# Kernel tuning notes

Measured on AMD Instinct MI355X. Metric: run time of the kernel, lower is better.

The kernel has to match this reference:

```python
import jax, jax.numpy as jnp
import numpy as np

IN, H, L, T = 44, 128, 4, 50  # input_size, hidden_size, num_layers, target_len
B, S = 2048, 200


def _lstm_cell(xt, h, c, Wih, Whh, b):
    # xt [B,in], h/c [B,H]; Wih [4H,in], Whh [4H,H], b [4H] (b_ih+b_hh fused)
    gates = xt @ Wih.T + h @ Whh.T + b
    i, f, g, o = jnp.split(gates, 4, axis=-1)
    c_new = jax.nn.sigmoid(f) * c + jax.nn.sigmoid(i) * jnp.tanh(g)
    h_new = jax.nn.sigmoid(o) * jnp.tanh(c_new)
    return h_new, c_new


def _run_layer(xs, Wih, Whh, b):
    # xs [S,B,in] -> ys [S,B,H], final (h,c)
    Bn = xs.shape[1]
    h0 = jnp.zeros((Bn, H), xs.dtype)
    c0 = jnp.zeros((Bn, H), xs.dtype)

    def step(carry, xt):
        h, c = carry
        h, c = _lstm_cell(xt, h, c, Wih, Whh, b)
        return (h, c), h

    (hT, cT), ys = jax.lax.scan(step, (h0, c0), xs)
    return ys, hT, cT


def setup_inputs() -> dict:
    key = jax.random.key(0)
    ks = jax.random.split(key, 16)
    s = 1.0 / np.sqrt(H)
    u = lambda k, shape: jax.random.uniform(k, shape, jnp.float32, -s, s)
    return {
        "x": jax.random.normal(ks[0], (B, S, IN), jnp.float32),
        "target": jax.random.normal(ks[1], (B, T, IN), jnp.float32),
        "enc_Wih0": u(ks[2], (4 * H, IN)),
        "enc_WihR": u(ks[3], (L - 1, 4 * H, H)),
        "enc_Whh": u(ks[4], (L, 4 * H, H)),
        "enc_b": u(ks[5], (L, 4 * H)),
        "dec_Wih0": u(ks[6], (4 * H, IN)),
        "dec_WihR": u(ks[7], (L - 1, 4 * H, H)),
        "dec_Whh": u(ks[8], (L, 4 * H, H)),
        "dec_b": u(ks[9], (L, 4 * H)),
        "fc_W": u(ks[10], (IN, H)),
        "fc_b": u(ks[11], (IN,)),
    }


def reference(x, target, enc_Wih0, enc_WihR, enc_Whh, enc_b,
              dec_Wih0, dec_WihR, dec_Whh, dec_b, fc_W, fc_b):
    # ---- encoder: 4-layer LSTM over the source sequence ----
    xs = jnp.transpose(x, (1, 0, 2))  # [S,B,IN]
    ys, h, c = _run_layer(xs, enc_Wih0, enc_Whh[0], enc_b[0])
    hs, cs = [h], [c]
    for l in range(1, L):
        ys, h, c = _run_layer(ys, enc_WihR[l - 1], enc_Whh[l], enc_b[l])
        hs.append(h)
        cs.append(c)
    hs = jnp.stack(hs)  # [L,B,H]
    cs = jnp.stack(cs)

    # ---- decoder: recursive decode for T steps (seq_len=1 per step) ----
    dec_in0 = x[:, -1, :]  # [B,IN]

    def dec_step(carry, _):
        dec_in, hsc, csc = carry
        new_h, new_c = [], []
        inp = dec_in
        for l in range(L):
            Wih = dec_Wih0 if l == 0 else dec_WihR[l - 1]
            hl, cl = _lstm_cell(inp, hsc[l], csc[l], Wih, dec_Whh[l], dec_b[l])
            new_h.append(hl)
            new_c.append(cl)
            inp = hl
        out = inp @ fc_W.T + fc_b  # [B,IN]
        return (out, jnp.stack(new_h), jnp.stack(new_c)), out

    _, outs = jax.lax.scan(dec_step, (dec_in0, hs, cs), None, length=T)
    return jnp.transpose(outs, (1, 0, 2))  # [B,T,IN]
```

## Files before the change

kernel.cpp:

```cpp
#include <hip/hip_runtime.h>
#include <hip/hip_bf16.h>
#include <cstdint>
#include <cstddef>

typedef _Float16 half8  __attribute__((ext_vector_type(8)));
typedef float    floatx4 __attribute__((ext_vector_type(4)));
typedef int      int4v   __attribute__((ext_vector_type(4)));

#define S_LEN 200
#define BATCH 2048
#define HID   128
#define T_LEN 50
#define IN_D  44

#define SENT32 0x7E007E00

#define OFF_ENCW   0ull
#define OFF_DECW   983040ull
#define OFF_RING_E 1978368ull
#define OFF_RING_D 14561280ull
#define OFF_ORING  20852736ull
#define OFF_HENC   21901312ull
#define OFF_CENC   23998464ull
#define OFF_FLAGS  28192768ull

#define SCOPE_AGENT __HIP_MEMORY_SCOPE_AGENT

#define LOG2E  1.44269504f
#define LOG2E2 2.88539008f
__device__ __forceinline__ float sigf(float x){
  float e = __builtin_amdgcn_exp2f(-LOG2E * x);
  return __builtin_amdgcn_rcpf(1.f + e);
}
__device__ __forceinline__ float tanhf_fast(float x){
  float e = __builtin_amdgcn_exp2f(LOG2E2 * x);
  return 1.f - 2.f * __builtin_amdgcn_rcpf(e + 1.f);
}

__device__ __forceinline__ int  ldc(const int* p){ return __hip_atomic_load(p, __ATOMIC_RELAXED, SCOPE_AGENT); }
__device__ __forceinline__ void stc(int* p, int v){ __hip_atomic_store(p, v, __ATOMIC_RELAXED, SCOPE_AGENT); }
__device__ __forceinline__ void drain_vm(){ asm volatile("s_waitcnt vmcnt(0)" ::: "memory"); }
__device__ __forceinline__ int* flagp(int* flags, int idx){ return flags + idx*32; }

__device__ __forceinline__ int4v ld_ring_x4(const int* p){
  int4v r;
  asm volatile("global_load_dwordx4 %0, %1, off sc0 sc1\n\t"
               "s_waitcnt vmcnt(0)"
               : "=v"(r) : "v"(p) : "memory");
  return r;
}
__device__ __forceinline__ void ld_ring_x4x2(int4v &r0, int4v &r1,
                                             const int* p0, const int* p1){
  asm volatile("global_load_dwordx4 %0, %2, off sc0 sc1\n\t"
               "global_load_dwordx4 %1, %3, off sc0 sc1\n\t"
               "s_waitcnt vmcnt(0)"
               : "=&v"(r0), "=&v"(r1)
               : "v"(p0), "v"(p1)
               : "memory");
}
__device__ __forceinline__ void st_ring_x4(int* p, int4v v){
  asm volatile("global_store_dwordx4 %0, %1, off sc0 sc1"
               :: "v"(p), "v"(v) : "memory");
}
__device__ __forceinline__ bool any_sent(int4v v){
  return (v.x==SENT32)||(v.y==SENT32)||(v.z==SENT32)||(v.w==SENT32);
}

#define PIN(v) asm volatile("" : "+v"(v))

__global__ void prep_weights(const float* __restrict__ eW0, const float* __restrict__ eWR,
                             const float* __restrict__ eWH, const float* __restrict__ dW0,
                             const float* __restrict__ dWR, const float* __restrict__ dWH,
                             const float* __restrict__ fcW,
                             _Float16* __restrict__ encw, _Float16* __restrict__ decw,
                             int* __restrict__ rings, int* __restrict__ flags)
{
  int i = blockIdx.x*256 + threadIdx.x;
  if (i < 491520) {
    _Float16 v;
    if (i < 32768)      { int j=i>>6, k=i&63; v = (k<IN_D)? (_Float16)eW0[j*IN_D+k] : (_Float16)0.f; }
    else if (i < 229376){ v = (_Float16)eWR[i-32768]; }
    else                { v = (_Float16)eWH[i-229376]; }
    encw[i] = v;
  }
  if (i < 497664) {
    _Float16 v;
    if (i < 32768)      { int j=i>>6, k=i&63; v = (k<IN_D)? (_Float16)dW0[j*IN_D+k] : (_Float16)0.f; }
    else if (i < 229376){ v = (_Float16)dWR[i-32768]; }
    else if (i < 491520){ v = (_Float16)dWH[i-229376]; }
    else { int r=i-491520; int j=r>>7, k=r&127; v = (j<IN_D)? (_Float16)fcW[j*HID+k] : (_Float16)0.f; }
    decw[i] = v;
  }
  for (int j = i; j < 4980736; j += 4096*256) rings[j] = SENT32;
  if (i < 32768) flags[i] = 0;
}


__global__ __launch_bounds__(512, 2)
void enc_pipe(const float* __restrict__ x, const _Float16* __restrict__ encw,
              const float* __restrict__ enc_b, _Float16* __restrict__ ring,
              _Float16* __restrict__ h_enc, float* __restrict__ c_enc,
              int* __restrict__ flags)
{
  const int tid = threadIdx.x;
  const int w = tid >> 6, lane = tid & 63, quad = lane >> 4, n16 = lane & 15;
  const int l = blockIdx.x >> 6, s = blockIdx.x & 63, r0 = s * 32;
  const int u = w*16 + n16;
  const int KSI = (l == 0) ? 2 : 4;
  const int my4 = tid*4;

  __shared__ _Float16 xb[2][32][136];
  __shared__ _Float16 hA[32][136];
  __shared__ _Float16 hB[32][136];

  for (int i = tid; i < 32*136; i += 512){
    ((_Float16*)xb[0])[i] = (_Float16)0.f;
    ((_Float16*)xb[1])[i] = (_Float16)0.f;
    ((_Float16*)hA)[i] = (_Float16)0.f;
    ((_Float16*)hB)[i] = (_Float16)0.f;
  }

  const _Float16* Wi = (l==0) ? encw : encw + 32768 + (size_t)(l-1)*65536;
  const _Float16* Wh = encw + 229376 + (size_t)l*65536;
  const int KI = KSI * 32;
  floatx4 wfi[4][4], wfh[4][4];
  #pragma unroll
  for (int nt = 0; nt < 4; ++nt){
    const int grow = nt*128 + u;
    #pragma unroll
    for (int ks = 0; ks < 4; ++ks){
      if (ks < KSI){ wfi[nt][ks] = *(const floatx4*)(Wi + (size_t)grow*KI + ks*32 + quad*8); PIN(wfi[nt][ks]); }
      wfh[nt][ks] = *(const floatx4*)(Wh + (size_t)grow*HID + ks*32 + quad*8); PIN(wfh[nt][ks]);
    }
  }
  float breg[4];
  #pragma unroll
  for (int g = 0; g < 4; ++g) breg[g] = enc_b[l*512 + g*128 + u];
  float creg[2][4] = {{0.f,0.f,0.f,0.f},{0.f,0.f,0.f,0.f}};

  int xr_r[3], xr_k[3]; bool xr_v[3]; float xr[2][3];
  if (l == 0){
    #pragma unroll
    for (int j = 0; j < 3; ++j){
      int idx = tid + j*512; xr_v[j] = idx < 32*IN_D;
      xr_r[j] = xr_v[j] ? idx / IN_D : 0; xr_k[j] = xr_v[j] ? idx % IN_D : 0;
      #pragma unroll
      for (int p = 0; p < 2; ++p)
        xr[p][j] = xr_v[j] ? x[((size_t)(r0+xr_r[j])*S_LEN + p)*IN_D + xr_k[j]] : 0.f;
    }
  }

  int* cflag_self = flagp(flags, l*64 + s);
  int* cflag_next = flagp(flags, (l+1)*64 + s);
  int seen_cons = 0;

  auto cell = [&](const _Float16 (*xin)[136], const _Float16 (*hin)[136],
                  _Float16 (*hout)[136], bool writeHC){
    #pragma unroll
    for (int m = 0; m < 2; ++m){
      half8 ai[4], ah[4];
      #pragma unroll
      for (int ks = 0; ks < 4; ++ks){
        if (ks < KSI) ai[ks] = *(const half8*)&xin[m*16+n16][ks*32 + quad*8];
        ah[ks] = *(const half8*)&hin[m*16+n16][ks*32 + quad*8];
      }
      floatx4 acc[4];
      #pragma unroll
      for (int nt = 0; nt < 4; ++nt){
        acc[nt] = (floatx4){0.f,0.f,0.f,0.f};
        #pragma unroll
        for (int ks = 0; ks < 4; ++ks){
          if (ks < KSI) acc[nt] = __builtin_amdgcn_mfma_f32_16x16x32_f16(ai[ks], __builtin_bit_cast(half8, wfi[nt][ks]), acc[nt], 0,0,0);
          acc[nt] = __builtin_amdgcn_mfma_f32_16x16x32_f16(ah[ks], __builtin_bit_cast(half8, wfh[nt][ks]), acc[nt], 0,0,0);
        }
      }
      #pragma unroll
      for (int rr = 0; rr < 4; ++rr){
        float ip = acc[0][rr] + breg[0];
        float fp = acc[1][rr] + breg[1];
        float gp = acc[2][rr] + breg[2];
        float op = acc[3][rr] + breg[3];
        float cc = sigf(fp)*creg[m][rr] + sigf(ip)*tanhf_fast(gp);
        float hh = sigf(op)*tanhf_fast(cc);
        creg[m][rr] = cc;
        const int row = m*16 + quad*4 + rr;
        hout[row][u] = (_Float16)hh;
        if (writeHC){
          h_enc[((size_t)l*BATCH + r0 + row)*HID + u] = (_Float16)hh;
          c_enc[((size_t)l*BATCH + r0 + row)*HID + u] = cc;
        }
      }
    }
  };

  __syncthreads();

  const int4v sv = {SENT32, SENT32, SENT32, SENT32};

  for (int q = 0; q < S_LEN/2; ++q){
    if (l == 0){
      #pragma unroll
      for (int p = 0; p < 2; ++p)
        #pragma unroll
        for (int j = 0; j < 3; ++j)
          if (xr_v[j]) xb[p][xr_r[j]][xr_k[j]] = (_Float16)xr[p][j];
    } else {
      const int sbase = (l-1)*8 + ((q&3)<<1);
      int* s0 = (int*)(ring + ((size_t)(sbase+0)*BATCH + r0)*HID) + my4;
      int* s1 = (int*)(ring + ((size_t)(sbase+1)*BATCH + r0)*HID) + my4;
      int4v v0, v1;
      ld_ring_x4x2(v0, v1, s0, s1);
      while (any_sent(v0)){ __builtin_amdgcn_s_sleep(1); v0 = ld_ring_x4(s0); }
      while (any_sent(v1)){ __builtin_amdgcn_s_sleep(1); v1 = ld_ring_x4(s1); }
      *(int4v*)&xb[0][my4>>6][(my4&63)*2] = v0;
      *(int4v*)&xb[1][my4>>6][(my4&63)*2] = v1;
      st_ring_x4(s0, sv);
      st_ring_x4(s1, sv);
    }
    if (tid == 0 && l < 3 && q >= 4){
      while (seen_cons < q-3){
        seen_cons = ldc(cflag_next);
        if (seen_cons < q-3) __builtin_amdgcn_s_sleep(1);
      }
    }
    __syncthreads();

    if (l == 0 && q < S_LEN/2 - 1){
      #pragma unroll
      for (int p = 0; p < 2; ++p)
        #pragma unroll
        for (int j = 0; j < 3; ++j)
          if (xr_v[j]) xr[p][j] = x[((size_t)(r0+xr_r[j])*S_LEN + (2*q+2+p))*IN_D + xr_k[j]];
    }

    cell(xb[0], hA, hB, false);
    __syncthreads();
    if (l < 3){
      const int dbase = l*8 + ((q&3)<<1);
      int* d0p = (int*)(ring + ((size_t)(dbase+0)*BATCH + r0)*HID) + my4;
      st_ring_x4(d0p, *(const int4v*)&hB[my4>>6][(my4&63)*2]);
    }
    cell(xb[1], hB, hA, (q == S_LEN/2 - 1));
    __syncthreads();

    if (l > 0){
      drain_vm();
      if (tid == 0) stc(cflag_self, q+1);
    }
    if (l < 3){
      const int dbase = l*8 + ((q&3)<<1);
      int* d1p = (int*)(ring + ((size_t)(dbase+1)*BATCH + r0)*HID) + my4;
      st_ring_x4(d1p, *(const int4v*)&hA[my4>>6][(my4&63)*2]);
    }
  }
  drain_vm();
}


__global__ __launch_bounds__(512, 2)
void dec_pipe(const float* __restrict__ x, const _Float16* __restrict__ decw,
              const float* __restrict__ dec_b, const float* __restrict__ fc_b,
              _Float16* __restrict__ ring, _Float16* __restrict__ oring,
              const _Float16* __restrict__ h_enc, const float* __restrict__ c_enc,
              int* __restrict__ flags, float* __restrict__ out)
{
  const int tid = threadIdx.x;
  const int w = tid >> 6, lane = tid & 63, quad = lane >> 4, n16 = lane & 15;
  const int l = blockIdx.x >> 6, s = blockIdx.x & 63, r0 = s * 32;
  const int u = w*16 + n16;
  const int KSI = (l == 0) ? 2 : 4;
  const int my4 = tid*4;

  __shared__ _Float16 xbuf[32][136];
  __shared__ _Float16 hb[2][32][136];
  __shared__ _Float16 fcout[32][64];

  for (int i = tid; i < 32*136; i += 512) ((_Float16*)xbuf)[i] = (_Float16)0.f;
  for (int i = tid; i < 32*64; i += 512) ((_Float16*)fcout)[i] = (_Float16)0.f;

  const _Float16* Wi = (l==0) ? decw : decw + 32768 + (size_t)(l-1)*65536;
  const _Float16* Wh = decw + 229376 + (size_t)l*65536;
  const _Float16* FCW = decw + 491520;
  const int KI = KSI * 32;
  floatx4 wfi[4][4], wfh[4][4];
  #pragma unroll
  for (int nt = 0; nt < 4; ++nt){
    const int grow = nt*128 + u;
    #pragma unroll
    for (int ks = 0; ks < 4; ++ks){
      if (ks < KSI){ wfi[nt][ks] = *(const floatx4*)(Wi + (size_t)grow*KI + ks*32 + quad*8); PIN(wfi[nt][ks]); }
      wfh[nt][ks] = *(const floatx4*)(Wh + (size_t)grow*HID + ks*32 + quad*8); PIN(wfh[nt][ks]);
    }
  }
  float breg[4];
  #pragma unroll
  for (int g = 0; g < 4; ++g) breg[g] = dec_b[l*512 + g*128 + u];

  {
    int idx = tid*8, rr_ = idx >> 7, kk = idx & 127;
    *(half8*)&hb[0][rr_][kk] = *(const half8*)(h_enc + ((size_t)l*BATCH + r0)*HID + rr_*HID + kk);
  }
  float creg[2][4];
  #pragma unroll
  for (int m = 0; m < 2; ++m)
    #pragma unroll
    for (int rr = 0; rr < 4; ++rr)
      creg[m][rr] = c_enc[((size_t)l*BATCH + r0 + m*16 + quad*4 + rr)*HID + u];

  floatx4 wfc[4]; float fcb_j = 0.f;
  const int j = w*16 + n16;
  if (w < 3){
    #pragma unroll
    for (int ks = 0; ks < 4; ++ks){
      wfc[ks] = *(const floatx4*)(FCW + (size_t)j*HID + ks*32 + quad*8); PIN(wfc[ks]);
    }
    if (j < IN_D) fcb_j = fc_b[j];
  }

  int* cflag_self = flagp(flags, 256 + l*64 + s);
  int* cflag_next = flagp(flags, 256 + (l+1)*64 + s);
  int* cflag_o    = flagp(flags, 512 + s);
  int seen = 0;

  __syncthreads();

  _Float16 (*hcur)[136] = hb[0];
  _Float16 (*hnxt)[136] = hb[1];

  const int4v sv = {SENT32, SENT32, SENT32, SENT32};

  for (int t = 0; t < T_LEN; ++t){
    if (l == 0){
      if (t == 0){
        for (int idx = tid; idx < 32*IN_D; idx += 512){
          int r = idx / IN_D, k = idx % IN_D;
          xbuf[r][k] = (_Float16)x[((size_t)(r0+r)*S_LEN + (S_LEN-1))*IN_D + k];
        }
      } else if (tid < 256){
        int* srcd = (int*)(oring + (((size_t)((t-1)&3))*BATCH + r0)*64);
        int4v v = ld_ring_x4(srcd + my4);
        while (any_sent(v)){
          __builtin_amdgcn_s_sleep(1);
          v = ld_ring_x4(srcd + my4);
        }
        *(int4v*)&xbuf[my4>>5][(my4&31)*2] = v;
        st_ring_x4(srcd + my4, sv);
      }
    } else {
      int* srcd = (int*)(ring + (((size_t)(l-1)*4 + (t&3))*BATCH + r0)*HID);
      int4v v = ld_ring_x4(srcd + my4);
      while (any_sent(v)){
        __builtin_amdgcn_s_sleep(1);
        v = ld_ring_x4(srcd + my4);
      }
      *(int4v*)&xbuf[my4>>6][(my4&63)*2] = v;
      st_ring_x4(srcd + my4, sv);
    }
    if (tid == 0 && t >= 4){
      if (l < 3){
        while (seen < t-3){ seen = ldc(cflag_next); if (seen < t-3) __builtin_amdgcn_s_sleep(1); }
      } else {
        while (seen < t-2){ seen = ldc(cflag_o); if (seen < t-2) __builtin_amdgcn_s_sleep(1); }
      }
    }
    __syncthreads();

    #pragma unroll
    for (int m = 0; m < 2; ++m){
      half8 ai[4], ah[4];
      #pragma unroll
      for (int ks = 0; ks < 4; ++ks){
        if (ks < KSI) ai[ks] = *(const half8*)&xbuf[m*16+n16][ks*32 + quad*8];
        ah[ks] = *(const half8*)&hcur[m*16+n16][ks*32 + quad*8];
      }
      floatx4 acc[4];
      #pragma unroll
      for (int nt = 0; nt < 4; ++nt){
        acc[nt] = (floatx4){0.f,0.f,0.f,0.f};
        #pragma unroll
        for (int ks = 0; ks < 4; ++ks){
          if (ks < KSI) acc[nt] = __builtin_amdgcn_mfma_f32_16x16x32_f16(ai[ks], __builtin_bit_cast(half8, wfi[nt][ks]), acc[nt], 0,0,0);
          acc[nt] = __builtin_amdgcn_mfma_f32_16x16x32_f16(ah[ks], __builtin_bit_cast(half8, wfh[nt][ks]), acc[nt], 0,0,0);
        }
      }
      #pragma unroll
      for (int rr = 0; rr < 4; ++rr){
        float ip = acc[0][rr] + breg[0];
        float fp = acc[1][rr] + breg[1];
        float gp = acc[2][rr] + breg[2];
        float op = acc[3][rr] + breg[3];
        float cc = sigf(fp)*creg[m][rr] + sigf(ip)*tanhf_fast(gp);
        float hh = sigf(op)*tanhf_fast(cc);
        creg[m][rr] = cc;
        hnxt[m*16 + quad*4 + rr][u] = (_Float16)hh;
      }
    }
    __syncthreads();

    drain_vm();
    if (tid == 0){
      if (l > 0) stc(cflag_self, t+1);
      else if (t > 0) stc(cflag_o, t+1);
    }

    if (l < 3){
      int* dst = (int*)(ring + (((size_t)l*4 + (t&3))*BATCH + r0)*HID);
      st_ring_x4(dst + my4, *(const int4v*)&hnxt[my4>>6][(my4&63)*2]);
    } else {
      if (w < 3){
        #pragma unroll
        for (int m = 0; m < 2; ++m){
          half8 a3[4];
          #pragma unroll
          for (int ks = 0; ks < 4; ++ks) a3[ks] = *(const half8*)&hnxt[m*16+n16][ks*32 + quad*8];
          floatx4 facc = (floatx4){0.f,0.f,0.f,0.f};
          #pragma unroll
          for (int ks = 0; ks < 4; ++ks) facc = __builtin_amdgcn_mfma_f32_16x16x32_f16(a3[ks], __builtin_bit_cast(half8, wfc[ks]), facc, 0,0,0);
          #pragma unroll
          for (int rr = 0; rr < 4; ++rr){
            const int row = m*16 + quad*4 + rr;
            float v = facc[rr] + fcb_j;
            fcout[row][j] = (_Float16)v;
            if (j < IN_D)
              out[((size_t)(r0 + row)*T_LEN + t)*IN_D + j] = v;
          }
        }
      }
      __syncthreads();
      if (tid < 256){
        int* odst = (int*)(oring + (((size_t)(t&3))*BATCH + r0)*64);
        st_ring_x4(odst + my4, *(const int4v*)&fcout[my4>>5][(my4&31)*2]);
      }
    }
    _Float16 (*tmp)[136] = hcur; hcur = hnxt; hnxt = tmp;
  }
  drain_vm();
}

extern "C" void kernel_launch(void* const* d_in, const int* in_sizes, int n_in,
                              void* d_out, int out_size, void* d_ws, size_t ws_size,
                              hipStream_t stream)
{
  const float* x        = (const float*)d_in[0];
  const float* enc_Wih0 = (const float*)d_in[2];
  const float* enc_WihR = (const float*)d_in[3];
  const float* enc_Whh  = (const float*)d_in[4];
  const float* enc_b    = (const float*)d_in[5];
  const float* dec_Wih0 = (const float*)d_in[6];
  const float* dec_WihR = (const float*)d_in[7];
  const float* dec_Whh  = (const float*)d_in[8];
  const float* dec_b    = (const float*)d_in[9];
  const float* fc_W     = (const float*)d_in[10];
  const float* fc_b     = (const float*)d_in[11];

  char* ws = (char*)d_ws;
  _Float16* encw   = (_Float16*)(ws + OFF_ENCW);
  _Float16* decw   = (_Float16*)(ws + OFF_DECW);
  _Float16* ring_e = (_Float16*)(ws + OFF_RING_E);
  _Float16* ring_d = (_Float16*)(ws + OFF_RING_D);
  _Float16* oring  = (_Float16*)(ws + OFF_ORING);
  _Float16* h_enc  = (_Float16*)(ws + OFF_HENC);
  float*    c_enc  = (float*)(ws + OFF_CENC);
  int*      flags  = (int*)(ws + OFF_FLAGS);
  int*      rings  = (int*)(ws + OFF_RING_E);
  float*    outp   = (float*)d_out;

  prep_weights<<<4096, 256, 0, stream>>>(enc_Wih0, enc_WihR, enc_Whh,
                                         dec_Wih0, dec_WihR, dec_Whh, fc_W,
                                         encw, decw, rings, flags);
  enc_pipe<<<256, 512, 0, stream>>>(x, encw, enc_b, ring_e, h_enc, c_enc, flags);
  dec_pipe<<<256, 512, 0, stream>>>(x, decw, dec_b, fc_b, ring_d, oring,
                                    h_enc, c_enc, flags, outp);
}
```

Before: 1.274 ms.

## Fuse pairs of decoder layers into one 1024-thread block

The decoder now runs two consecutive LSTM layers inside one 1024-thread block, 128 blocks instead of 256. The inner layer's hidden state passes through shared memory instead of the global ring. Backpressure flags are dropped, and the ring between layer 1 and layer 2 is the only remaining cross-block handoff besides the output ring. This aims to cut global-ring traffic and spin-wait latency on the serial decode chain, at the cost of serialising the two layers within a block with extra __syncthreads. The launch bound of (1024,4) may also squeeze registers that hold pinned weights.

```diff
diff --git a/kernel.cpp b/kernel.cpp
--- a/kernel.cpp
+++ b/kernel.cpp
@@ -135,7 +135,7 @@
   }
   float breg[4];
   #pragma unroll
-  for (int g = 0; g < 4; ++g) breg[g] = enc_b[l*512 + g*128 + u];
+  for (int gg = 0; gg < 4; ++gg) breg[gg] = enc_b[l*512 + gg*128 + u];
   float creg[2][4] = {{0.f,0.f,0.f,0.f},{0.f,0.f,0.f,0.f}};
 
   int xr_r[3], xr_k[3]; bool xr_v[3]; float xr[2][3];
@@ -257,26 +257,30 @@
 }
 
 
-__global__ __launch_bounds__(512, 2)
+__global__ __launch_bounds__(1024, 4)
 void dec_pipe(const float* __restrict__ x, const _Float16* __restrict__ decw,
               const float* __restrict__ dec_b, const float* __restrict__ fc_b,
               _Float16* __restrict__ ring, _Float16* __restrict__ oring,
               const _Float16* __restrict__ h_enc, const float* __restrict__ c_enc,
               int* __restrict__ flags, float* __restrict__ out)
 {
-  const int tid = threadIdx.x;
-  const int w = tid >> 6, lane = tid & 63, quad = lane >> 4, n16 = lane & 15;
-  const int l = blockIdx.x >> 6, s = blockIdx.x & 63, r0 = s * 32;
+  (void)flags;
+  const int tid  = threadIdx.x;
+  const int g    = tid >> 9;
+  const int stid = tid & 511;
+  const int w = stid >> 6, lane = stid & 63, quad = lane >> 4, n16 = lane & 15;
+  const int pair = blockIdx.x >> 6, s = blockIdx.x & 63, r0 = s * 32;
+  const int l = pair*2 + g;
   const int u = w*16 + n16;
   const int KSI = (l == 0) ? 2 : 4;
-  const int my4 = tid*4;
-
-  __shared__ _Float16 xbuf[32][136];
-  __shared__ _Float16 hb[2][32][136];
+  const int my4 = stid*4;
+
+  __shared__ _Float16 xin[32][136];
+  __shared__ _Float16 hs[2][2][32][136];
   __shared__ _Float16 fcout[32][64];
 
-  for (int i = tid; i < 32*136; i += 512) ((_Float16*)xbuf)[i] = (_Float16)0.f;
-  for (int i = tid; i < 32*64; i += 512) ((_Float16*)fcout)[i] = (_Float16)0.f;
+  for (int i = tid; i < 32*136; i += 1024) ((_Float16*)xin)[i] = (_Float16)0.f;
+  for (int i = tid; i < 32*64;  i += 1024) ((_Float16*)fcout)[i] = (_Float16)0.f;
 
   const _Float16* Wi = (l==0) ? decw : decw + 32768 + (size_t)(l-1)*65536;
   const _Float16* Wh = decw + 229376 + (size_t)l*65536;
@@ -294,11 +298,11 @@
   }
   float breg[4];
   #pragma unroll
-  for (int g = 0; g < 4; ++g) breg[g] = dec_b[l*512 + g*128 + u];
+  for (int gg = 0; gg < 4; ++gg) breg[gg] = dec_b[l*512 + gg*128 + u];
 
   {
-    int idx = tid*8, rr_ = idx >> 7, kk = idx & 127;
-    *(half8*)&hb[0][rr_][kk] = *(const half8*)(h_enc + ((size_t)l*BATCH + r0)*HID + rr_*HID + kk);
+    int idx = stid*8, rr_ = idx >> 7, kk = idx & 127;
+    *(half8*)&hs[g][1][rr_][kk] = *(const half8*)(h_enc + ((size_t)l*BATCH + r0)*HID + rr_*HID + kk);
   }
   float creg[2][4];
   #pragma unroll
@@ -308,8 +312,8 @@
       creg[m][rr] = c_enc[((size_t)l*BATCH + r0 + m*16 + quad*4 + rr)*HID + u];
 
   floatx4 wfc[4]; float fcb_j = 0.f;
-  const int j = w*16 + n16;
-  if (w < 3){
+  const int j = u;
+  if (pair == 1 && g == 1 && w < 3){
     #pragma unroll
     for (int ks = 0; ks < 4; ++ks){
       wfc[ks] = *(const floatx4*)(FCW + (size_t)j*HID + ks*32 + quad*8); PIN(wfc[ks]);
@@ -317,61 +321,15 @@
     if (j < IN_D) fcb_j = fc_b[j];
   }
 
-  int* cflag_self = flagp(flags, 256 + l*64 + s);
-  int* cflag_next = flagp(flags, 256 + (l+1)*64 + s);
-  int* cflag_o    = flagp(flags, 512 + s);
-  int seen = 0;
-
-  __syncthreads();
-
-  _Float16 (*hcur)[136] = hb[0];
-  _Float16 (*hnxt)[136] = hb[1];
-
-  const int4v sv = {SENT32, SENT32, SENT32, SENT32};
-
-  for (int t = 0; t < T_LEN; ++t){
-    if (l == 0){
-      if (t == 0){
-        for (int idx = tid; idx < 32*IN_D; idx += 512){
-          int r = idx / IN_D, k = idx % IN_D;
-          xbuf[r][k] = (_Float16)x[((size_t)(r0+r)*S_LEN + (S_LEN-1))*IN_D + k];
-        }
-      } else if (tid < 256){
-        int* srcd = (int*)(oring + (((size_t)((t-1)&3))*BATCH + r0)*64);
-        int4v v = ld_ring_x4(srcd + my4);
-        while (any_sent(v)){
-          __builtin_amdgcn_s_sleep(1);
-          v = ld_ring_x4(srcd + my4);
-        }
-        *(int4v*)&xbuf[my4>>5][(my4&31)*2] = v;
-        st_ring_x4(srcd + my4, sv);
-      }
-    } else {
-      int* srcd = (int*)(ring + (((size_t)(l-1)*4 + (t&3))*BATCH + r0)*HID);
-      int4v v = ld_ring_x4(srcd + my4);
-      while (any_sent(v)){
-        __builtin_amdgcn_s_sleep(1);
-        v = ld_ring_x4(srcd + my4);
-      }
-      *(int4v*)&xbuf[my4>>6][(my4&63)*2] = v;
-      st_ring_x4(srcd + my4, sv);
-    }
-    if (tid == 0 && t >= 4){
-      if (l < 3){
-        while (seen < t-3){ seen = ldc(cflag_next); if (seen < t-3) __builtin_amdgcn_s_sleep(1); }
-      } else {
-        while (seen < t-2){ seen = ldc(cflag_o); if (seen < t-2) __builtin_amdgcn_s_sleep(1); }
-      }
-    }
-    __syncthreads();
-
+  auto cell = [&](const _Float16 (*xinb)[136], const _Float16 (*hin)[136],
+                  _Float16 (*hout)[136]){
     #pragma unroll
     for (int m = 0; m < 2; ++m){
       half8 ai[4], ah[4];
       #pragma unroll
       for (int ks = 0; ks < 4; ++ks){
-        if (ks < KSI) ai[ks] = *(const half8*)&xbuf[m*16+n16][ks*32 + quad*8];
-        ah[ks] = *(const half8*)&hcur[m*16+n16][ks*32 + quad*8];
+        if (ks < KSI) ai[ks] = *(const half8*)&xinb[m*16+n16][ks*32 + quad*8];
+        ah[ks] = *(const half8*)&hin[m*16+n16][ks*32 + quad*8];
       }
       floatx4 acc[4];
       #pragma unroll
@@ -392,27 +350,61 @@
         float cc = sigf(fp)*creg[m][rr] + sigf(ip)*tanhf_fast(gp);
         float hh = sigf(op)*tanhf_fast(cc);
         creg[m][rr] = cc;
-        hnxt[m*16 + quad*4 + rr][u] = (_Float16)hh;
-      }
-    }
-    __syncthreads();
-
+        hout[m*16 + quad*4 + rr][u] = (_Float16)hh;
+      }
+    }
+  };
+
+  __syncthreads();
+
+  const int4v sv = {SENT32, SENT32, SENT32, SENT32};
+
+  for (int t = 0; t < T_LEN; ++t){
+    const int tb = t & 1, pb = tb ^ 1;
+
+    if (g == 0){
+      if (pair == 0){
+        if (t == 0){
+          for (int idx = stid; idx < 32*IN_D; idx += 512){
+            int r = idx / IN_D, k = idx % IN_D;
+            xin[r][k] = (_Float16)x[((size_t)(r0+r)*S_LEN + (S_LEN-1))*IN_D + k];
+          }
+        } else if (stid < 256){
+          int* srcd = (int*)(oring + (((size_t)((t-1)&3))*BATCH + r0)*64);
+          int4v v = ld_ring_x4(srcd + my4);
+          while (any_sent(v)){ __builtin_amdgcn_s_sleep(1); v = ld_ring_x4(srcd + my4); }
+          *(int4v*)&xin[my4>>5][(my4&31)*2] = v;
+          st_ring_x4(srcd + my4, sv);
+        }
+      } else {
+        int* srcd = (int*)(ring + (((size_t)(t&3))*BATCH + r0)*HID);
+        int4v v = ld_ring_x4(srcd + my4);
+        while (any_sent(v)){ __builtin_amdgcn_s_sleep(1); v = ld_ring_x4(srcd + my4); }
+        *(int4v*)&xin[my4>>6][(my4&63)*2] = v;
+        st_ring_x4(srcd + my4, sv);
+      }
+    }
+    __syncthreads();
+
+    if (g == 0) cell(xin, hs[0][pb], hs[0][tb]);
+    __syncthreads();
+
+    if (g == 1) cell(hs[0][tb], hs[1][pb], hs[1][tb]);
     drain_vm();
-    if (tid == 0){
-      if (l > 0) stc(cflag_self, t+1);
-      else if (t > 0) stc(cflag_o, t+1);
-    }
-
-    if (l < 3){
-      int* dst = (int*)(ring + (((size_t)l*4 + (t&3))*BATCH + r0)*HID);
-      st_ring_x4(dst + my4, *(const int4v*)&hnxt[my4>>6][(my4&63)*2]);
+    __syncthreads();
+
+    if (pair == 0){
+      if (g == 0){
+        int* dst = (int*)(ring + (((size_t)(t&3))*BATCH + r0)*HID);
+        st_ring_x4(dst + my4, *(const int4v*)&hs[1][tb][my4>>6][(my4&63)*2]);
+      }
     } else {
-      if (w < 3){
+      if (g == 1 && w < 3){
         #pragma unroll
         for (int m = 0; m < 2; ++m){
           half8 a3[4];
           #pragma unroll
-          for (int ks = 0; ks < 4; ++ks) a3[ks] = *(const half8*)&hnxt[m*16+n16][ks*32 + quad*8];
+          for (int ks = 0; ks < 4; ++ks) a3[ks] = *(const half8*)&hs[1][tb][m*16+n16][ks*32 + quad*8];
           floatx4 facc = (floatx4){0.f,0.f,0.f,0.f};
           #pragma unroll
           for (int ks = 0; ks < 4; ++ks) facc = __builtin_amdgcn_mfma_f32_16x16x32_f16(a3[ks], __builtin_bit_cast(half8, wfc[ks]), facc, 0,0,0);
@@ -426,13 +418,12 @@
           }
         }
       }
-      __syncthreads();
-      if (tid < 256){
-        int* odst = (int*)(oring + (((size_t)(t&3))*BATCH + r0)*64);
-        st_ring_x4(odst + my4, *(const int4v*)&fcout[my4>>5][(my4&31)*2]);
-      }
-    }
-    _Float16 (*tmp)[136] = hcur; hcur = hnxt; hnxt = tmp;
+    }
+    __syncthreads();
+    if (pair == 1 && g == 0 && stid < 256){
+      int* odst = (int*)(oring + (((size_t)(t&3))*BATCH + r0)*64);
+      st_ring_x4(odst + my4, *(const int4v*)&fcout[my4>>5][(my4&31)*2]);
+    }
   }
   drain_vm();
 }
@@ -469,6 +460,6 @@
                                          dec_Wih0, dec_WihR, dec_Whh, fc_W,
                                          encw, decw, rings, flags);
   enc_pipe<<<256, 512, 0, stream>>>(x, encw, enc_b, ring_e, h_enc, c_enc, flags);
-  dec_pipe<<<256, 512, 0, stream>>>(x, decw, dec_b, fc_b, ring_d, oring,
-                                    h_enc, c_enc, flags, outp);
-}
+  dec_pipe<<<128, 1024, 0, stream>>>(x, decw, dec_b, fc_b, ring_d, oring,
+                                     h_enc, c_enc, flags, outp);
+}
```

Result: slower. 2.791 ms (+119.0%).
